# Kernel tuning notes

Measured on AMD Instinct MI355X. Metric: run time of the kernel, lower is better.

## Reference

```python
import jax, jax.numpy as jnp
import numpy as np

N_NODES = 100000
N_EDGES = 800000
D_DATA = 100
H_DIM = 256
N_CLS = 47
K = 10
ALPHA = 0.1


def setup_inputs() -> dict:
    key = jax.random.key(0)
    ks = jax.random.split(key, 7)
    x = jax.random.normal(ks[0], (N_NODES, D_DATA), dtype=jnp.float32)
    src = jax.random.randint(ks[1], (N_EDGES,), 0, N_NODES, dtype=jnp.int32)
    dst = jax.random.randint(ks[2], (N_EDGES,), 0, N_NODES, dtype=jnp.int32)
    W1 = jax.random.normal(ks[3], (D_DATA, H_DIM), dtype=jnp.float32) / np.sqrt(D_DATA)
    b1 = jax.random.normal(ks[4], (H_DIM,), dtype=jnp.float32) * 0.01
    W2 = jax.random.normal(ks[5], (H_DIM, N_CLS), dtype=jnp.float32) / np.sqrt(H_DIM)
    b2 = jax.random.normal(ks[6], (N_CLS,), dtype=jnp.float32) * 0.01
    return {"x": x, "src": src, "dst": dst, "W1": W1, "b1": b1, "W2": W2, "b2": b2}


def reference(x, src, dst, W1, b1, W2, b2):
    # --- APPNPConv: K steps of symmetric-normalized SpMM + teleport ---
    # DGL normalizes with in-degree^{-1/2} on both message source and output.
    deg = jax.ops.segment_sum(jnp.ones((N_EDGES,), x.dtype), dst, num_segments=N_NODES)
    norm = jax.lax.rsqrt(jnp.maximum(deg, 1.0))[:, None]  # [N,1]
    h = x
    for _ in range(K):
        msg = (h * norm)[src]                              # gather src feats, [E,D]
        agg = jax.ops.segment_sum(msg, dst, num_segments=N_NODES)
        h = (1.0 - ALPHA) * (agg * norm) + ALPHA * x
    # --- feat_trans MLP (dropout inactive in eval) ---
    z = jax.nn.relu(h @ W1 + b1)
    logits = z @ W2 + b2
    return logits
```

## Files before the change

kernel.cpp:

```cpp
#include <hip/hip_runtime.h>
#include <hip/hip_fp16.h>


#define N_NODES 100000
#define N_PAD   100032
#define N_EDGES 800000
#define D_DATA  100
#define H_DIM   256
#define N_CLS   47
#define K_STEPS 10
#define ALPHA   0.1f
#define HS      128
#define MB      64

#define SCAN_NB    200
#define SCAN_CHUNK 500
#define EW_CAP (N_EDGES + 7 * N_NODES)

typedef _Float16 half8_t __attribute__((ext_vector_type(8)));
typedef float floatx4 __attribute__((ext_vector_type(4)));


__global__ void deg_kernel(const int* __restrict__ dst, int* __restrict__ deg,
                           int* __restrict__ slot, int e) {
    int i = blockIdx.x * blockDim.x + threadIdx.x;
    if (i < e) slot[i] = atomicAdd(&deg[dst[i]], 1);
}

__global__ __launch_bounds__(256) void scan_partial_kernel(
        const int* __restrict__ deg, int* __restrict__ partials) {
    __shared__ int red[256];
    int t = threadIdx.x;
    int base = blockIdx.x * SCAN_CHUNK;
    int s = 0;
    int i0 = 2 * t, i1 = 2 * t + 1;
    if (i0 < SCAN_CHUNK) s += (deg[base + i0] + 7) & ~7;
    if (i1 < SCAN_CHUNK) s += (deg[base + i1] + 7) & ~7;
    red[t] = s;
    __syncthreads();
    for (int off = 128; off > 0; off >>= 1) {
        if (t < off) red[t] += red[t + off];
        __syncthreads();
    }
    if (t == 0) partials[blockIdx.x] = red[0];
}

__global__ __launch_bounds__(256) void scan_top_kernel(
        const int* __restrict__ partials, int* __restrict__ pofs,
        int* __restrict__ row_ptr) {
    __shared__ int s[256];
    int t = threadIdx.x;
    s[t] = (t < SCAN_NB) ? partials[t] : 0;
    __syncthreads();
    for (int off = 1; off < 256; off <<= 1) {
        int v = (t >= off) ? s[t - off] : 0;
        __syncthreads();
        s[t] += v;
        __syncthreads();
    }
    if (t < SCAN_NB) pofs[t] = s[t] - partials[t];
    if (t == SCAN_NB - 1) row_ptr[N_NODES] = s[t];
}

__global__ __launch_bounds__(256) void scan_emit_kernel(
        const int* __restrict__ deg, const int* __restrict__ pofs,
        int* __restrict__ row_ptr, float* __restrict__ norm) {
    __shared__ int s[256];
    int t = threadIdx.x;
    int base = blockIdx.x * SCAN_CHUNK;
    int i0 = 2 * t, i1 = 2 * t + 1;
    int d0 = (i0 < SCAN_CHUNK) ? deg[base + i0] : 0;
    int d1 = (i1 < SCAN_CHUNK) ? deg[base + i1] : 0;
    int p0 = (d0 + 7) & ~7, p1 = (d1 + 7) & ~7;
    s[t] = p0 + p1;
    __syncthreads();
    for (int off = 1; off < 256; off <<= 1) {
        int v = (t >= off) ? s[t - off] : 0;
        __syncthreads();
        s[t] += v;
        __syncthreads();
    }
    int p = s[t] - (p0 + p1) + pofs[blockIdx.x];
    if (i0 < SCAN_CHUNK) {
        row_ptr[base + i0] = p;
        norm[base + i0] = rsqrtf((float)max(d0, 1));
    }
    if (i1 < SCAN_CHUNK) {
        row_ptr[base + i1] = p + p0;
        norm[base + i1] = rsqrtf((float)max(d1, 1));
    }
}

__global__ void scatter_kernel(const int* __restrict__ src, const int* __restrict__ dst,
                               const int* __restrict__ slot,
                               const int* __restrict__ row_ptr,
                               int* __restrict__ es, int e) {
    int i = blockIdx.x * blockDim.x + threadIdx.x;
    if (i < e) es[row_ptr[dst[i]] + slot[i]] = src[i];
}

__global__ void pad_kernel(const int* __restrict__ deg, const int* __restrict__ row_ptr,
                           int* __restrict__ es, int n) {
    int i = blockIdx.x * blockDim.x + threadIdx.x;
    if (i < n) {
        int b = row_ptr[i] + deg[i];
        int e = row_ptr[i + 1];
        for (int s = b; s < e; ++s) es[s] = N_NODES;
    }
}

__global__ void pack_w1_kernel(const float* __restrict__ W1, __half* __restrict__ W1p) {
    int idx = blockIdx.x * blockDim.x + threadIdx.x;
    if (idx >= 16 * 4 * 64 * 8) return;
    int j = idx & 7;
    int lane = (idx >> 3) & 63;
    int ks = (idx >> 9) & 3;
    int nt = idx >> 11;
    int k = ks * 32 + (lane >> 4) * 8 + j;
    int n = nt * 16 + (lane & 15);
    float v = (k < D_DATA) ? W1[(size_t)k * H_DIM + n] : 0.f;
    W1p[idx] = __float2half(v);
}

__global__ void pack_w2_kernel(const float* __restrict__ W2, __half* __restrict__ W2p) {
    int idx = blockIdx.x * blockDim.x + threadIdx.x;
    if (idx >= 3 * 8 * 64 * 8) return;
    int j = idx & 7;
    int lane = (idx >> 3) & 63;
    int ks = (idx >> 9) & 7;
    int nt = idx >> 12;
    int k = ks * 32 + (lane >> 4) * 8 + j;
    int n = nt * 16 + (lane & 15);
    float v = (n < N_CLS) ? W2[(size_t)k * N_CLS + n] : 0.f;
    W2p[idx] = __float2half(v);
}

__global__ void convert_xhat_kernel(const float* __restrict__ x,
                                    const float* __restrict__ norm,
                                    __half2* __restrict__ xh, int n_half2) {
    int i = blockIdx.x * blockDim.x + threadIdx.x;
    if (i < n_half2) {
        int node = i >> 6;
        int c2 = i & 63;
        float2 v = make_float2(0.f, 0.f);
        if (node < N_NODES && c2 < D_DATA / 2) {
            float nn = norm[node];
            const float2* r = (const float2*)(x + (size_t)node * D_DATA);
            float2 xv = r[c2];
            v = make_float2(nn * xv.x, nn * xv.y);
        }
        xh[i] = __float22half2_rn(v);
    }
}

__global__ void zero_rows_kernel(__half2* __restrict__ a, __half2* __restrict__ b) {
    int i = threadIdx.x;
    if (i < 64) a[(size_t)N_NODES * (HS / 2) + i] = __half2();
    else        b[(size_t)N_NODES * (HS / 2) + (i - 64)] = __half2();
}


template <bool FINAL>
__global__ __launch_bounds__(256) void prop_kernel(
        const __half* __restrict__ hin, const __half* __restrict__ xhat,
        const float* __restrict__ xf,
        const float* __restrict__ norm, const int* __restrict__ row_ptr,
        const int* __restrict__ es, __half* __restrict__ hout, int n_nodes) {
    int lane = threadIdx.x & 63;
    int wave = blockIdx.x * 4 + (threadIdx.x >> 6);
    int nA = __builtin_amdgcn_readfirstlane(wave * 2);
    if (nA >= n_nodes) return;
    int nB = nA + 1;
    int begA = __builtin_amdgcn_readfirstlane(row_ptr[nA]);
    int begB = __builtin_amdgcn_readfirstlane(row_ptr[nB]);
    int endB = __builtin_amdgcn_readfirstlane(row_ptr[nB + 1]);
    int nbA = (begB - begA) >> 3;
    int nbB = (endB - begB) >> 3;
    int mb = nbA > nbB ? nbA : nbB;

    float a0x = 0.f, a0y = 0.f, a1x = 0.f, a1y = 0.f;
    float b0x = 0.f, b0y = 0.f, b1x = 0.f, b1y = 0.f;
    for (int it = 0; it < mb; ++it) {
        bool doA = it < nbA, doB = it < nbB;
        int sA[8], sB[8];
        if (doA) {
            int e = begA + it * 8;
#pragma unroll
            for (int j = 0; j < 8; ++j) sA[j] = es[e + j];
        }
        if (doB) {
            int e = begB + it * 8;
#pragma unroll
            for (int j = 0; j < 8; ++j) sB[j] = es[e + j];
        }
        __half2 hvA[8], hvB[8];
        if (doA) {
#pragma unroll
            for (int j = 0; j < 8; ++j)
                hvA[j] = ((const __half2*)(hin + (size_t)sA[j] * HS))[lane];
        }
        if (doB) {
#pragma unroll
            for (int j = 0; j < 8; ++j)
                hvB[j] = ((const __half2*)(hin + (size_t)sB[j] * HS))[lane];
        }
        if (doA) {
            float2 v0 = __half22float2(hvA[0]), v1 = __half22float2(hvA[1]);
            float2 v2 = __half22float2(hvA[2]), v3 = __half22float2(hvA[3]);
            float2 v4 = __half22float2(hvA[4]), v5 = __half22float2(hvA[5]);
            float2 v6 = __half22float2(hvA[6]), v7 = __half22float2(hvA[7]);
            a0x += (v0.x + v2.x) + (v4.x + v6.x);
            a0y += (v0.y + v2.y) + (v4.y + v6.y);
            a1x += (v1.x + v3.x) + (v5.x + v7.x);
            a1y += (v1.y + v3.y) + (v5.y + v7.y);
        }
        if (doB) {
            float2 v0 = __half22float2(hvB[0]), v1 = __half22float2(hvB[1]);
            float2 v2 = __half22float2(hvB[2]), v3 = __half22float2(hvB[3]);
            float2 v4 = __half22float2(hvB[4]), v5 = __half22float2(hvB[5]);
            float2 v6 = __half22float2(hvB[6]), v7 = __half22float2(hvB[7]);
            b0x += (v0.x + v2.x) + (v4.x + v6.x);
            b0y += (v0.y + v2.y) + (v4.y + v6.y);
            b1x += (v1.x + v3.x) + (v5.x + v7.x);
            b1y += (v1.y + v3.y) + (v5.y + v7.y);
        }
    }
    {
        if (!FINAL) {
            float nn = norm[nA];
            float c = (1.0f - ALPHA) * nn * nn;
            float2 t = __half22float2(((const __half2*)(xhat + (size_t)nA * HS))[lane]);
            float2 o = make_float2(c * (a0x + a1x) + ALPHA * t.x,
                                   c * (a0y + a1y) + ALPHA * t.y);
            ((__half2*)(hout + (size_t)nA * HS))[lane] = __float22half2_rn(o);
        } else {
            float c = (1.0f - ALPHA) * norm[nA];
            float2 xv = make_float2(0.f, 0.f);
            if (lane < D_DATA / 2)
                xv = ((const float2*)(xf + (size_t)nA * D_DATA))[lane];
            float2 o = make_float2(c * (a0x + a1x) + ALPHA * xv.x,
                                   c * (a0y + a1y) + ALPHA * xv.y);
            ((__half2*)(hout + (size_t)nA * HS))[lane] = __float22half2_rn(o);
        }
    }
    {
        if (!FINAL) {
            float nn = norm[nB];
            float c = (1.0f - ALPHA) * nn * nn;
            float2 t = __half22float2(((const __half2*)(xhat + (size_t)nB * HS))[lane]);
            float2 o = make_float2(c * (b0x + b1x) + ALPHA * t.x,
                                   c * (b0y + b1y) + ALPHA * t.y);
            ((__half2*)(hout + (size_t)nB * HS))[lane] = __float22half2_rn(o);
        } else {
            float c = (1.0f - ALPHA) * norm[nB];
            float2 xv = make_float2(0.f, 0.f);
            if (lane < D_DATA / 2)
                xv = ((const float2*)(xf + (size_t)nB * D_DATA))[lane];
            float2 o = make_float2(c * (b0x + b1x) + ALPHA * xv.x,
                                   c * (b0y + b1y) + ALPHA * xv.y);
            ((__half2*)(hout + (size_t)nB * HS))[lane] = __float22half2_rn(o);
        }
    }
}


#define ZP 264

__global__ __launch_bounds__(256, 4) void mlp_mfma_kernel(
        const __half* __restrict__ h16,
        const __half* __restrict__ W1p, const float* __restrict__ b1,
        const __half* __restrict__ W2p, const float* __restrict__ b2,
        float* __restrict__ out, int n_nodes) {
    __shared__ _Float16 zs[MB][ZP];
    int tid = threadIdx.x;
    int lane = tid & 63;
    int w = tid >> 6;
    int q = lane >> 4;
    int r = lane & 15;
    int node0 = blockIdx.x * MB + w * 16;

    half8_t a1[4];
#pragma unroll
    for (int ks = 0; ks < 4; ++ks)
        a1[ks] = *(const half8_t*)(h16 + (size_t)(node0 + r) * HS + ks * 32 + q * 8);

    const half8_t* w1f = (const half8_t*)W1p;
#pragma unroll 4
    for (int nt = 0; nt < 16; ++nt) {
        floatx4 acc = {0.f, 0.f, 0.f, 0.f};
#pragma unroll
        for (int ks = 0; ks < 4; ++ks) {
            half8_t b = w1f[(nt * 4 + ks) * 64 + lane];
            acc = __builtin_amdgcn_mfma_f32_16x16x32_f16(a1[ks], b, acc, 0, 0, 0);
        }
        float bb = b1[nt * 16 + r];
#pragma unroll
        for (int reg = 0; reg < 4; ++reg) {
            float zv = fmaxf(acc[reg] + bb, 0.f);
            zs[w * 16 + q * 4 + reg][nt * 16 + r] = (_Float16)zv;
        }
    }

    half8_t a2[8];
#pragma unroll
    for (int ks = 0; ks < 8; ++ks)
        a2[ks] = *(const half8_t*)&zs[w * 16 + r][ks * 32 + q * 8];

    const half8_t* w2f = (const half8_t*)W2p;
#pragma unroll
    for (int nt = 0; nt < 3; ++nt) {
        floatx4 acc = {0.f, 0.f, 0.f, 0.f};
#pragma unroll
        for (int ks = 0; ks < 8; ++ks) {
            half8_t b = w2f[(nt * 8 + ks) * 64 + lane];
            acc = __builtin_amdgcn_mfma_f32_16x16x32_f16(a2[ks], b, acc, 0, 0, 0);
        }
        int cix = nt * 16 + r;
        if (cix < N_CLS) {
            float bb = b2[cix];
#pragma unroll
            for (int reg = 0; reg < 4; ++reg) {
                int node = node0 + q * 4 + reg;
                if (node < n_nodes)
                    out[(size_t)node * N_CLS + cix] = acc[reg] + bb;
            }
        }
    }
}


static inline size_t align_up(size_t v, size_t a) { return (v + a - 1) & ~(a - 1); }

extern "C" void kernel_launch(void* const* d_in, const int* in_sizes, int n_in,
                              void* d_out, int out_size, void* d_ws, size_t ws_size,
                              hipStream_t stream) {
    const float* x   = (const float*)d_in[0];
    const int*   src = (const int*)d_in[1];
    const int*   dst = (const int*)d_in[2];
    const float* W1  = (const float*)d_in[3];
    const float* b1  = (const float*)d_in[4];
    const float* W2  = (const float*)d_in[5];
    const float* b2  = (const float*)d_in[6];
    float* out = (float*)d_out;

    char* p = (char*)d_ws;
    size_t off = 0;
    int* deg = (int*)(p + off);           off = align_up(off + N_NODES * 4, 256);
    int* row_ptr = (int*)(p + off);       off = align_up(off + (N_NODES + 1) * 4, 256);
    int* slot = (int*)(p + off);          off = align_up(off + (size_t)N_EDGES * 4, 256);
    float* norm = (float*)(p + off);      off = align_up(off + N_NODES * 4, 256);
    int* partials = (int*)(p + off);      off = align_up(off + SCAN_NB * 4, 256);
    int* pofs = (int*)(p + off);          off = align_up(off + SCAN_NB * 4, 256);
    __half* W1p = (__half*)(p + off);     off = align_up(off + 16 * 4 * 64 * 8 * 2, 256);
    __half* W2p = (__half*)(p + off);     off = align_up(off + 3 * 8 * 64 * 8 * 2, 256);
    int* es = (int*)(p + off);            off = align_up(off + (size_t)EW_CAP * 4, 256);
    __half* xhat = (__half*)(p + off);    off = align_up(off + (size_t)N_PAD * HS * 2, 256);
    __half* h16A = (__half*)(p + off);    off = align_up(off + (size_t)N_PAD * HS * 2, 256);
    __half* h16B = (__half*)(p + off);    off = align_up(off + (size_t)N_PAD * HS * 2, 256);
    (void)ws_size;

    hipMemsetAsync(deg, 0, N_NODES * 4, stream);

    int eb = (N_EDGES + 255) / 256;
    deg_kernel<<<eb, 256, 0, stream>>>(dst, deg, slot, N_EDGES);
    scan_partial_kernel<<<SCAN_NB, 256, 0, stream>>>(deg, partials);
    scan_top_kernel<<<1, 256, 0, stream>>>(partials, pofs, row_ptr);
    scan_emit_kernel<<<SCAN_NB, 256, 0, stream>>>(deg, pofs, row_ptr, norm);
    scatter_kernel<<<eb, 256, 0, stream>>>(src, dst, slot, row_ptr, es, N_EDGES);
    pad_kernel<<<(N_NODES + 255) / 256, 256, 0, stream>>>(deg, row_ptr, es, N_NODES);
    pack_w1_kernel<<<128, 256, 0, stream>>>(W1, W1p);
    pack_w2_kernel<<<48, 256, 0, stream>>>(W2, W2p);

    int nh2 = (N_NODES + 1) * (HS / 2);
    convert_xhat_kernel<<<(nh2 + 255) / 256, 256, 0, stream>>>(x, norm, (__half2*)xhat, nh2);
    zero_rows_kernel<<<1, 128, 0, stream>>>((__half2*)h16A, (__half2*)h16B);

    int pb = (N_NODES / 2) / 4;
    prop_kernel<false><<<pb, 256, 0, stream>>>(xhat, xhat, nullptr, norm, row_ptr, es, h16A, N_NODES);
    const __half* hin = h16A;
    for (int k = 1; k < K_STEPS - 1; ++k) {
        __half* ho = (k & 1) ? h16B : h16A;
        prop_kernel<false><<<pb, 256, 0, stream>>>(hin, xhat, nullptr, norm, row_ptr, es, ho, N_NODES);
        hin = ho;
    }
    prop_kernel<true><<<pb, 256, 0, stream>>>(hin, nullptr, x, norm, row_ptr, es, h16B, N_NODES);

    int mbk = (N_NODES + MB - 1) / MB;
    mlp_mfma_kernel<<<mbk, 256, 0, stream>>>(h16B, W1p, b1, W2p, b2, out, N_NODES);
}
```

Before: 556.7 us.

## Split propagation features into two 64-wide slabs processed by separate grid halves

Propagation state moves from one 128-wide fp16 row per node into two slabs of 64 features each, and each propagation launch uses a 2-D grid with one half per slab. Each half-wave gathers a 128-byte row segment for alternating edges, and the two halves are combined with a cross-lane shuffle. The intent is a smaller working set per slab, which should give better L2 locality for the random gathers. In exchange, the edge index lists are read twice and twice as many blocks are launched. The final step writes a 128-wide row layout for the MLP, and the padding rows are zeroed per slab.

Measured after the change: 969.6 us. +74.2%, slower.

```diff
diff --git a/kernel.cpp b/kernel.cpp
--- a/kernel.cpp
+++ b/kernel.cpp
@@ -11,7 +11,10 @@
 #define K_STEPS 10
 #define ALPHA   0.1f
 #define HS      128
+#define SH      64
 #define MB      64
+
+#define SLAB_HALFS ((size_t)N_PAD * SH)
 
 #define SCAN_NB    200
 #define SCAN_CHUNK 500
@@ -137,36 +140,47 @@
 
 __global__ void convert_xhat_kernel(const float* __restrict__ x,
                                     const float* __restrict__ norm,
-                                    __half2* __restrict__ xh, int n_half2) {
+                                    __half2* __restrict__ xh) {
     int i = blockIdx.x * blockDim.x + threadIdx.x;
-    if (i < n_half2) {
-        int node = i >> 6;
-        int c2 = i & 63;
-        float2 v = make_float2(0.f, 0.f);
-        if (node < N_NODES && c2 < D_DATA / 2) {
-            float nn = norm[node];
-            const float2* r = (const float2*)(x + (size_t)node * D_DATA);
-            float2 xv = r[c2];
-            v = make_float2(nn * xv.x, nn * xv.y);
-        }
-        xh[i] = __float22half2_rn(v);
-    }
-}
-
-__global__ void zero_rows_kernel(__half2* __restrict__ a, __half2* __restrict__ b) {
-    int i = threadIdx.x;
-    if (i < 64) a[(size_t)N_NODES * (HS / 2) + i] = __half2();
-    else        b[(size_t)N_NODES * (HS / 2) + (i - 64)] = __half2();
+    if (i >= (N_NODES + 1) * (SH / 2)) return;
+    int slab = blockIdx.y;
+    int node = i >> 5;
+    int c = i & 31;
+    int f = slab * SH + 2 * c;
+    float2 v = make_float2(0.f, 0.f);
+    if (node < N_NODES && f <= D_DATA - 2) {
+        float nn = norm[node];
+        float2 xv = *(const float2*)(x + (size_t)node * D_DATA + f);
+        v = make_float2(nn * xv.x, nn * xv.y);
+    }
+    xh[(size_t)slab * (SLAB_HALFS / 2) + i] = __float22half2_rn(v);
+}
+
+__global__ void zero_misc_kernel(__half2* __restrict__ a, __half2* __restrict__ b,
+                                 __half2* __restrict__ h128) {
+    int t = threadIdx.x;
+    if (t < 32)        a[(size_t)N_NODES * 32 + t] = __half2();
+    else if (t < 64)   a[SLAB_HALFS / 2 + (size_t)N_NODES * 32 + (t - 32)] = __half2();
+    else if (t < 96)   b[(size_t)N_NODES * 32 + (t - 64)] = __half2();
+    else if (t < 128)  b[SLAB_HALFS / 2 + (size_t)N_NODES * 32 + (t - 96)] = __half2();
+    for (int i = t; i < 32 * (HS / 2); i += 256)
+        h128[(size_t)N_NODES * (HS / 2) + i] = __half2();
 }
 
 
 template <bool FINAL>
-__global__ __launch_bounds__(256) void prop_kernel(
-        const __half* __restrict__ hin, const __half* __restrict__ xhat,
+__global__ __launch_bounds__(256) void prop_half_kernel(
+        const __half* __restrict__ hin,
+        const __half* __restrict__ xh,
         const float* __restrict__ xf,
         const float* __restrict__ norm, const int* __restrict__ row_ptr,
         const int* __restrict__ es, __half* __restrict__ hout, int n_nodes) {
     int lane = threadIdx.x & 63;
+    int g = lane >> 5;
+    int c = lane & 31;
+    int slab = blockIdx.y;
+    const __half* hin_s = hin + (size_t)slab * SLAB_HALFS;
+
     int wave = blockIdx.x * 4 + (threadIdx.x >> 6);
     int nA = __builtin_amdgcn_readfirstlane(wave * 2);
     if (nA >= n_nodes) return;
@@ -178,8 +192,7 @@
     int nbB = (endB - begB) >> 3;
     int mb = nbA > nbB ? nbA : nbB;
 
-    float a0x = 0.f, a0y = 0.f, a1x = 0.f, a1y = 0.f;
-    float b0x = 0.f, b0y = 0.f, b1x = 0.f, b1y = 0.f;
+    float aAx = 0.f, aAy = 0.f, aBx = 0.f, aBy = 0.f;
     for (int it = 0; it < mb; ++it) {
         bool doA = it < nbA, doB = it < nbB;
         int sA[8], sB[8];
@@ -193,73 +206,58 @@
 #pragma unroll
             for (int j = 0; j < 8; ++j) sB[j] = es[e + j];
         }
-        __half2 hvA[8], hvB[8];
+        __half2 hvA[4], hvB[4];
         if (doA) {
 #pragma unroll
-            for (int j = 0; j < 8; ++j)
-                hvA[j] = ((const __half2*)(hin + (size_t)sA[j] * HS))[lane];
+            for (int t = 0; t < 4; ++t) {
+                int row = g ? sA[2 * t + 1] : sA[2 * t];
+                hvA[t] = ((const __half2*)(hin_s + (size_t)row * SH))[c];
+            }
         }
         if (doB) {
 #pragma unroll
-            for (int j = 0; j < 8; ++j)
-                hvB[j] = ((const __half2*)(hin + (size_t)sB[j] * HS))[lane];
+            for (int t = 0; t < 4; ++t) {
+                int row = g ? sB[2 * t + 1] : sB[2 * t];
+                hvB[t] = ((const __half2*)(hin_s + (size_t)row * SH))[c];
+            }
         }
         if (doA) {
             float2 v0 = __half22float2(hvA[0]), v1 = __half22float2(hvA[1]);
             float2 v2 = __half22float2(hvA[2]), v3 = __half22float2(hvA[3]);
-            float2 v4 = __half22float2(hvA[4]), v5 = __half22float2(hvA[5]);
-            float2 v6 = __half22float2(hvA[6]), v7 = __half22float2(hvA[7]);
-            a0x += (v0.x + v2.x) + (v4.x + v6.x);
-            a0y += (v0.y + v2.y) + (v4.y + v6.y);
-            a1x += (v1.x + v3.x) + (v5.x + v7.x);
-            a1y += (v1.y + v3.y) + (v5.y + v7.y);
+            aAx += (v0.x + v1.x) + (v2.x + v3.x);
+            aAy += (v0.y + v1.y) + (v2.y + v3.y);
         }
         if (doB) {
             float2 v0 = __half22float2(hvB[0]), v1 = __half22float2(hvB[1]);
             float2 v2 = __half22float2(hvB[2]), v3 = __half22float2(hvB[3]);
-            float2 v4 = __half22float2(hvB[4]), v5 = __half22float2(hvB[5]);
-            float2 v6 = __half22float2(hvB[6]), v7 = __half22float2(hvB[7]);
-            b0x += (v0.x + v2.x) + (v4.x + v6.x);
-            b0y += (v0.y + v2.y) + (v4.y + v6.y);
-            b1x += (v1.x + v3.x) + (v5.x + v7.x);
-            b1y += (v1.y + v3.y) + (v5.y + v7.y);
-        }
-    }
-    {
-        if (!FINAL) {
-            float nn = norm[nA];
-            float c = (1.0f - ALPHA) * nn * nn;
-            float2 t = __half22float2(((const __half2*)(xhat + (size_t)nA * HS))[lane]);
-            float2 o = make_float2(c * (a0x + a1x) + ALPHA * t.x,
-                                   c * (a0y + a1y) + ALPHA * t.y);
-            ((__half2*)(hout + (size_t)nA * HS))[lane] = __float22half2_rn(o);
-        } else {
-            float c = (1.0f - ALPHA) * norm[nA];
-            float2 xv = make_float2(0.f, 0.f);
-            if (lane < D_DATA / 2)
-                xv = ((const float2*)(xf + (size_t)nA * D_DATA))[lane];
-            float2 o = make_float2(c * (a0x + a1x) + ALPHA * xv.x,
-                                   c * (a0y + a1y) + ALPHA * xv.y);
-            ((__half2*)(hout + (size_t)nA * HS))[lane] = __float22half2_rn(o);
-        }
-    }
-    {
-        if (!FINAL) {
-            float nn = norm[nB];
-            float c = (1.0f - ALPHA) * nn * nn;
-            float2 t = __half22float2(((const __half2*)(xhat + (size_t)nB * HS))[lane]);
-            float2 o = make_float2(c * (b0x + b1x) + ALPHA * t.x,
-                                   c * (b0y + b1y) + ALPHA * t.y);
-            ((__half2*)(hout + (size_t)nB * HS))[lane] = __float22half2_rn(o);
-        } else {
-            float c = (1.0f - ALPHA) * norm[nB];
-            float2 xv = make_float2(0.f, 0.f);
-            if (lane < D_DATA / 2)
-                xv = ((const float2*)(xf + (size_t)nB * D_DATA))[lane];
-            float2 o = make_float2(c * (b0x + b1x) + ALPHA * xv.x,
-                                   c * (b0y + b1y) + ALPHA * xv.y);
-            ((__half2*)(hout + (size_t)nB * HS))[lane] = __float22half2_rn(o);
-        }
+            aBx += (v0.x + v1.x) + (v2.x + v3.x);
+            aBy += (v0.y + v1.y) + (v2.y + v3.y);
+        }
+    }
+    aAx += __shfl_xor(aAx, 32, 64);
+    aAy += __shfl_xor(aAy, 32, 64);
+    aBx += __shfl_xor(aBx, 32, 64);
+    aBy += __shfl_xor(aBy, 32, 64);
+
+    int node = g ? nB : nA;
+    float sx = g ? aBx : aAx;
+    float sy = g ? aBy : aAy;
+    if (!FINAL) {
+        float nn = norm[node];
+        float cf = (1.0f - ALPHA) * nn * nn;
+        float2 t = __half22float2(
+            ((const __half2*)(xh + (size_t)slab * SLAB_HALFS + (size_t)node * SH))[c]);
+        float2 o = make_float2(cf * sx + ALPHA * t.x, cf * sy + ALPHA * t.y);
+        ((__half2*)(hout + (size_t)slab * SLAB_HALFS + (size_t)node * SH))[c] =
+            __float22half2_rn(o);
+    } else {
+        float cf = (1.0f - ALPHA) * norm[node];
+        int f = slab * SH + 2 * c;
+        float2 xv = make_float2(0.f, 0.f);
+        if (f <= D_DATA - 2)
+            xv = *(const float2*)(xf + (size_t)node * D_DATA + f);
+        float2 o = make_float2(cf * sx + ALPHA * xv.x, cf * sy + ALPHA * xv.y);
+        ((__half2*)(hout + (size_t)node * HS + slab * SH))[c] = __float22half2_rn(o);
     }
 }
 
@@ -354,9 +352,10 @@
     __half* W1p = (__half*)(p + off);     off = align_up(off + 16 * 4 * 64 * 8 * 2, 256);
     __half* W2p = (__half*)(p + off);     off = align_up(off + 3 * 8 * 64 * 8 * 2, 256);
     int* es = (int*)(p + off);            off = align_up(off + (size_t)EW_CAP * 4, 256);
-    __half* xhat = (__half*)(p + off);    off = align_up(off + (size_t)N_PAD * HS * 2, 256);
-    __half* h16A = (__half*)(p + off);    off = align_up(off + (size_t)N_PAD * HS * 2, 256);
-    __half* h16B = (__half*)(p + off);    off = align_up(off + (size_t)N_PAD * HS * 2, 256);
+    __half* xhp = (__half*)(p + off);     off = align_up(off + 2 * SLAB_HALFS * 2, 256);
+    __half* hAA = (__half*)(p + off);     off = align_up(off + 2 * SLAB_HALFS * 2, 256);
+    __half* hBB = (__half*)(p + off);     off = align_up(off + 2 * SLAB_HALFS * 2, 256);
+    __half* h16 = (__half*)(p + off);     off = align_up(off + (size_t)N_PAD * HS * 2, 256);
     (void)ws_size;
 
     hipMemsetAsync(deg, 0, N_NODES * 4, stream);
@@ -371,20 +370,21 @@
     pack_w1_kernel<<<128, 256, 0, stream>>>(W1, W1p);
     pack_w2_kernel<<<48, 256, 0, stream>>>(W2, W2p);
 
-    int nh2 = (N_NODES + 1) * (HS / 2);
-    convert_xhat_kernel<<<(nh2 + 255) / 256, 256, 0, stream>>>(x, norm, (__half2*)xhat, nh2);
-    zero_rows_kernel<<<1, 128, 0, stream>>>((__half2*)h16A, (__half2*)h16B);
-
-    int pb = (N_NODES / 2) / 4;
-    prop_kernel<false><<<pb, 256, 0, stream>>>(xhat, xhat, nullptr, norm, row_ptr, es, h16A, N_NODES);
-    const __half* hin = h16A;
+    int nch = (N_NODES + 1) * (SH / 2);
+    convert_xhat_kernel<<<dim3((nch + 255) / 256, 2), 256, 0, stream>>>(
+        x, norm, (__half2*)xhp);
+    zero_misc_kernel<<<1, 256, 0, stream>>>((__half2*)hAA, (__half2*)hBB, (__half2*)h16);
+
+    dim3 pg((N_NODES / 2) / 4, 2);
+    prop_half_kernel<false><<<pg, 256, 0, stream>>>(xhp, xhp, nullptr, norm, row_ptr, es, hAA, N_NODES);
+    const __half* hin = hAA;
     for (int k = 1; k < K_STEPS - 1; ++k) {
-        __half* ho = (k & 1) ? h16B : h16A;
-        prop_kernel<false><<<pb, 256, 0, stream>>>(hin, xhat, nullptr, norm, row_ptr, es, ho, N_NODES);
+        __half* ho = (k & 1) ? hBB : hAA;
+        prop_half_kernel<false><<<pg, 256, 0, stream>>>(hin, xhp, nullptr, norm, row_ptr, es, ho, N_NODES);
         hin = ho;
     }
-    prop_kernel<true><<<pb, 256, 0, stream>>>(hin, nullptr, x, norm, row_ptr, es, h16B, N_NODES);
+    prop_half_kernel<true><<<pg, 256, 0, stream>>>(hin, nullptr, x, norm, row_ptr, es, h16, N_NODES);
 
     int mbk = (N_NODES + MB - 1) / MB;
-    mlp_mfma_kernel<<<mbk, 256, 0, stream>>>(h16B, W1p, b1, W2p, b2, out, N_NODES);
-}
+    mlp_mfma_kernel<<<mbk, 256, 0, stream>>>(h16, W1p, b1, W2p, b2, out, N_NODES);
+}
```
